# Optimization experiments

Hardware: AMD Instinct MI355X
Metric: run time of the kernel (lower is better)

## Reference

```python
import jax, jax.numpy as jnp
import numpy as np

K = 40  # GravNetConv k (hardcoded in PFNet7.forward's conv1)

def lrelu(x):
    # LeakyReLU(negative_slope=0.5)
    return jnp.where(x >= 0, x, 0.5 * x)

def lin(x, W, b=None):
    y = x @ W
    return y + b if b is not None else y


def setup_inputs() -> dict:
    key = jax.random.key(0)
    ks = jax.random.split(key, 24)
    N = 16384
    inp = {}
    inp["x0"] = jax.random.normal(ks[0], (N, 12), jnp.float32)
    inp["ygen"] = jax.random.normal(ks[1], (N, 6), jnp.float32)
    inp["ycand"] = jax.random.normal(ks[2], (N, 6), jnp.float32)
    inp["ygen_id"] = jax.random.randint(ks[3], (N,), 0, 6)
    inp["ycand_id"] = jax.random.randint(ks[4], (N,), 0, 6)

    def lp(k, din, dout):  # torch Linear default init (uniform +/- 1/sqrt(fan_in))
        s = float(1.0 / np.sqrt(din))
        kw, kb = jax.random.split(k)
        W = jax.random.uniform(kw, (din, dout), jnp.float32, -s, s)
        b = jax.random.uniform(kb, (dout,), jnp.float32, -s, s)
        return W, b

    inp["n1W0"], inp["n1b0"] = lp(ks[5], 12, 64)
    inp["n1W1"], inp["n1b1"] = lp(ks[6], 64, 64)
    inp["n1W2"], inp["n1b2"] = lp(ks[7], 64, 12)
    # GravNetConv: lin_s (space, 8), lin_h (propagate, 22), lin_out (12 + 2*22 -> 64)
    inp["gWs"], inp["gbs"] = lp(ks[8], 12, 8)
    inp["gWh"], inp["gbh"] = lp(ks[9], 12, 22)
    inp["gWo"], inp["gbo"] = lp(ks[10], 56, 64)
    # GraphConv: lin_rel (with bias), lin_root (no bias, PyG convention)
    inp["c2Wrel"], inp["c2brel"] = lp(ks[11], 64, 64)
    inp["c2Wroot"] = lp(ks[12], 64, 64)[0]
    inp["n2W0"], inp["n2b0"] = lp(ks[13], 64, 126)
    inp["n2W1"], inp["n2b1"] = lp(ks[14], 126, 126)
    inp["n2W2"], inp["n2b2"] = lp(ks[15], 126, 126)
    inp["n2W3"], inp["n2b3"] = lp(ks[16], 126, 6)
    inp["n3W0"], inp["n3b0"] = lp(ks[17], 82, 126)
    inp["n3W1"], inp["n3b1"] = lp(ks[18], 126, 126)
    inp["n3W2"], inp["n3b2"] = lp(ks[19], 126, 126)
    inp["n3W3"], inp["n3b3"] = lp(ks[20], 126, 6)
    return inp


def reference(x0, ygen, ycand, ygen_id, ycand_id,
              n1W0, n1b0, n1W1, n1b1, n1W2, n1b2,
              gWs, gbs, gWh, gbh, gWo, gbo,
              c2Wrel, c2brel, c2Wroot,
              n2W0, n2b0, n2W1, n2b1, n2W2, n2b2, n2W3, n2b3,
              n3W0, n3b0, n3W1, n3b1, n3W2, n3b2, n3W3, n3b3):
    N = x0.shape[0]
    # nn1 encoder
    x = lrelu(lin(x0, n1W0, n1b0))
    x = lrelu(lin(x, n1W1, n1b1))
    x = lrelu(lin(x, n1W2, n1b2))            # [N,12]
    # ---- GravNetConv: dynamic kNN graph in learned 8-dim space ----
    s = lin(x, gWs, gbs)                     # [N,8] spatial coords
    h = lin(x, gWh, gbh)                     # [N,22] propagated features
    sq = jnp.sum(s * s, axis=1)
    d2 = sq[:, None] + sq[None, :] - 2.0 * (s @ s.T)   # [N,N] squared dists
    ar = jnp.arange(N)
    d2 = d2.at[ar, ar].set(jnp.inf)          # knn_graph loop=False: no self edges
    negd2, idx = jax.lax.top_k(-d2, K)       # [N,K] k nearest neighbors
    w = jnp.exp(10.0 * negd2)                # edge_weight = exp(-10 * d^2)
    msg = h[idx] * w[..., None]              # [N,K,22] gathered messages
    agg = jnp.concatenate([msg.mean(axis=1), msg.max(axis=1)], axis=-1)  # [N,44]
    x = lin(jnp.concatenate([agg, x], axis=-1), gWo, gbo)  # [N,64]
    # ---- GraphConv on the same kNN graph (add-aggregation, edge-weighted) ----
    nbr = jnp.sum(x[idx] * w[..., None], axis=1)  # [N,64]
    x = lin(nbr, c2Wrel, c2brel) + x @ c2Wroot     # [N,64]
    # nn2: class id head
    y = lrelu(lin(x, n2W0, n2b0))
    y = lrelu(lin(y, n2W1, n2b1))
    y = lrelu(lin(y, n2W2, n2b2))
    cand_ids = lrelu(lin(y, n2W3, n2b3))     # [N,6]
    z = jnp.concatenate([x, cand_ids, x0], axis=-1)  # [N,82]
    z = lrelu(lin(z, n3W0, n3b0))
    z = lrelu(lin(z, n3W1, n3b1))
    z = lrelu(lin(z, n3W2, n3b2))
    cand_p4 = lrelu(lin(z, n3W3, n3b3))      # [N,6]
    return (cand_ids, cand_p4, ygen_id, ygen, ycand_id, ycand)
```

## Files before the change

### kernel.cpp

```cpp
#include <hip/hip_runtime.h>
#include <math.h>

static constexpr int KNN = 40;

__device__ __forceinline__ float lrelu_f(float v){ return v >= 0.f ? v : 0.5f*v; }

typedef _Float16 half8 __attribute__((ext_vector_type(8)));
typedef float    f32x4 __attribute__((ext_vector_type(4)));

__device__ __forceinline__ void gload16(const void* g, void* l){
    __builtin_amdgcn_global_load_lds((const __attribute__((address_space(1))) void*)g,
                                     (__attribute__((address_space(3))) void*)l, 16, 0, 0);
}

#define PAD_OFF_GWS   0
#define PAD_OFF_GWH   192
#define PAD_OFF_N1W2  576
#define PAD_OFF_N2W3  1600
#define PAD_OFF_N3W3  3616
#define PAD_TOTAL     5632

#define T_N2W0  0
#define T_N2W1  8192
#define T_N2W2  24576
#define T_N3W0  40960
#define T_N3W1  53248
#define T_N3W2  69632
#define T_TOTAL 86016

__global__ void pad_all(const float* gWs,const float* gWh,const float* n1W2,
                        const float* n2W3,const float* n3W3,
                        const float* n2W0,const float* n2W1,const float* n2W2,
                        const float* n3W0,const float* n3W1,const float* n3W2,
                        float* __restrict__ wp, _Float16* __restrict__ wt)
{
    int i = blockIdx.x*blockDim.x + threadIdx.x;
    if (i < PAD_TOTAL) {
        const float* src; int cols, sh, off;
        if      (i < PAD_OFF_GWH)  { src=gWs;  cols=8;  sh=4; off=PAD_OFF_GWS;  }
        else if (i < PAD_OFF_N1W2) { src=gWh;  cols=22; sh=5; off=PAD_OFF_GWH;  }
        else if (i < PAD_OFF_N2W3) { src=n1W2; cols=12; sh=4; off=PAD_OFF_N1W2; }
        else if (i < PAD_OFF_N3W3) { src=n2W3; cols=6;  sh=4; off=PAD_OFF_N2W3; }
        else                       { src=n3W3; cols=6;  sh=4; off=PAD_OFF_N3W3; }
        int li = i - off;
        int r = li >> sh, c = li & ((1<<sh)-1);
        wp[i] = (c < cols) ? src[r*cols + c] : 0.f;
        return;
    }
    int j = i - PAD_TOTAL;
    if (j >= T_TOTAL) return;
    const float* src; int KP, K, off;
    if      (j < T_N2W1) { src=n2W0; KP=64;  K=64;  off=T_N2W0; }
    else if (j < T_N2W2) { src=n2W1; KP=128; K=126; off=T_N2W1; }
    else if (j < T_N3W0) { src=n2W2; KP=128; K=126; off=T_N2W2; }
    else if (j < T_N3W1) { src=n3W0; KP=96;  K=82;  off=T_N3W0; }
    else if (j < T_N3W2) { src=n3W1; KP=128; K=126; off=T_N3W1; }
    else                 { src=n3W2; KP=128; K=126; off=T_N3W2; }
    int li = j - off;
    int n = li / KP, k = li - n*KP;
    float v = (n < 126 && k < K) ? src[k*126 + n] : 0.f;
    wt[j] = (_Float16)v;
}

template<int K, int NOUT, int WPITCH, bool RELU, int NTH>
__device__ __forceinline__
void lin8(const float* __restrict__ Xs, int xpitch,
          const float* __restrict__ W, const float* __restrict__ Bv,
          float* __restrict__ Y, int ypitch, int tid)
{
    constexpr int NP  = ((NOUT+7)/8)*8;
    constexpr int NCG = NP/8;
    constexpr int NW  = NTH/64;
    const int lane = tid & 63;
    for (int g0 = tid >> 6; g0 < NCG; g0 += NW) {
        const int cg = __builtin_amdgcn_readfirstlane(g0);
        float acc[8];
        #pragma unroll
        for (int j=0;j<8;++j){ int c=cg*8+j; acc[j] = (c < NOUT) ? Bv[c] : 0.f; }
        const float* xrow = &Xs[(long)lane*xpitch];
        const float* wp = &W[cg*8];
        #pragma unroll 4
        for (int k=0;k<K;++k){
            const float xv = xrow[k];
            const float4* w4 = reinterpret_cast<const float4*>(wp + (long)k*WPITCH);
            float4 a = w4[0], b = w4[1];
            acc[0]=fmaf(xv,a.x,acc[0]); acc[1]=fmaf(xv,a.y,acc[1]);
            acc[2]=fmaf(xv,a.z,acc[2]); acc[3]=fmaf(xv,a.w,acc[3]);
            acc[4]=fmaf(xv,b.x,acc[4]); acc[5]=fmaf(xv,b.y,acc[5]);
            acc[6]=fmaf(xv,b.z,acc[6]); acc[7]=fmaf(xv,b.w,acc[7]);
        }
        #pragma unroll
        for (int j=0;j<8;++j){
            int c = cg*8 + j;
            if (c < NOUT){ float v = acc[j]; if (RELU) v = lrelu_f(v); Y[(long)lane*ypitch + c] = v; }
        }
    }
    __syncthreads();
}

template<int K, int NOUT, int WPITCH, int NTH>
__device__ __forceinline__
void lin8_dual(const float* __restrict__ Xs, int xp, const float* __restrict__ X2s, int xp2,
               const float* __restrict__ W, const float* __restrict__ Bv, const float* __restrict__ W2,
               float* __restrict__ Y, int ypitch, int tid)
{
    constexpr int NP  = ((NOUT+7)/8)*8;
    constexpr int NCG = NP/8;
    constexpr int NW  = NTH/64;
    const int lane = tid & 63;
    for (int g0 = tid >> 6; g0 < NCG; g0 += NW) {
        const int cg = __builtin_amdgcn_readfirstlane(g0);
        float acc[8];
        #pragma unroll
        for (int j=0;j<8;++j){ int c=cg*8+j; acc[j] = (c < NOUT) ? Bv[c] : 0.f; }
        {
            const float* xrow = &Xs[(long)lane*xp];
            const float* wp = &W[cg*8];
            #pragma unroll 4
            for (int k=0;k<K;++k){
                const float xv = xrow[k];
                const float4* w4 = reinterpret_cast<const float4*>(wp + (long)k*WPITCH);
                float4 a = w4[0], b = w4[1];
                acc[0]=fmaf(xv,a.x,acc[0]); acc[1]=fmaf(xv,a.y,acc[1]);
                acc[2]=fmaf(xv,a.z,acc[2]); acc[3]=fmaf(xv,a.w,acc[3]);
                acc[4]=fmaf(xv,b.x,acc[4]); acc[5]=fmaf(xv,b.y,acc[5]);
                acc[6]=fmaf(xv,b.z,acc[6]); acc[7]=fmaf(xv,b.w,acc[7]);
            }
        }
        {
            const float* xrow = &X2s[(long)lane*xp2];
            const float* wp = &W2[cg*8];
            #pragma unroll 4
            for (int k=0;k<K;++k){
                const float xv = xrow[k];
                const float4* w4 = reinterpret_cast<const float4*>(wp + (long)k*WPITCH);
                float4 a = w4[0], b = w4[1];
                acc[0]=fmaf(xv,a.x,acc[0]); acc[1]=fmaf(xv,a.y,acc[1]);
                acc[2]=fmaf(xv,a.z,acc[2]); acc[3]=fmaf(xv,a.w,acc[3]);
                acc[4]=fmaf(xv,b.x,acc[4]); acc[5]=fmaf(xv,b.y,acc[5]);
                acc[6]=fmaf(xv,b.z,acc[6]); acc[7]=fmaf(xv,b.w,acc[7]);
            }
        }
        #pragma unroll
        for (int j=0;j<8;++j){
            int c = cg*8 + j;
            if (c < NOUT) Y[(long)lane*ypitch + c] = acc[j];
        }
    }
    __syncthreads();
}

__global__ __launch_bounds__(256)
void f1_encoder(const float* __restrict__ x0, const float* __restrict__ wp,
                const float* n1W0,const float* n1b0,const float* n1W1,const float* n1b1,
                const float* n1b2, const float* gbs, const float* gbh,
                float* __restrict__ x12g,
                _Float16* __restrict__ SA16, _Float16* __restrict__ SB16 ,
                float* __restrict__ hg )
{
    __shared__ float A1[64*65], A2[64*65], Ss[64*9];
    const int tid = threadIdx.x;
    const long row0 = (long)blockIdx.x*64;
    lin8<12,64,64,true,256>(x0+row0*12,12, n1W0, n1b0, A1,65, tid);
    lin8<64,64,64,true,256>(A1,65, n1W1, n1b1, A2,65, tid);
    lin8<64,12,16,true,256>(A2,65, wp+PAD_OFF_N1W2, n1b2, A1,13, tid);
    for (int i=tid;i<64*12;i+=256){ int r=i/12,c=i-r*12; x12g[(row0+r)*12+c]=A1[r*13+c]; }
    lin8<12,8,16,false,256>(A1,13, wp+PAD_OFF_GWS, gbs, Ss,9, tid);
    lin8<12,22,32,false,256>(A1,13, wp+PAD_OFF_GWH, gbh, hg+row0*32,32, tid);
    if (tid < 64) {
        const long node = row0 + tid;
        float sv[8]; float nq = 0.f;
        #pragma unroll
        for (int k=0;k<8;++k){ float v=Ss[tid*9+k]; sv[k]=v; nq=fmaf(v,v,nq); }
        _Float16 ch[8], clo[8];
        #pragma unroll
        for (int k=0;k<8;++k){ ch[k]=(_Float16)sv[k]; clo[k]=(_Float16)(sv[k]-(float)ch[k]); }
        _Float16 nh = (_Float16)nq, nl = (_Float16)(nq-(float)nh);
        const _Float16 one = (_Float16)1.f, zero = (_Float16)0.f;
        half8 a0,a1,a2,b0,b2;
        #pragma unroll
        for (int k=0;k<8;++k){
            a0[k]=ch[k]; a1[k]=clo[k]; a2[k]=ch[k];
            b0[k]=(_Float16)(-2.f*(float)ch[k]);
            b2[k]=(_Float16)(-2.f*(float)clo[k]);
        }
        half8 a3 = {nh, nl, one, one, zero, zero, zero, zero};
        half8 b3 = {one, one, nh, nl, zero, zero, zero, zero};
        half8* ap = (half8*)&SA16[(size_t)node*32];
        ap[0]=a0; ap[1]=a1; ap[2]=a2; ap[3]=a3;
        half8* bp = (half8*)&SB16[(size_t)node*40];
        bp[0]=b0; bp[1]=b0; bp[2]=b2; bp[3]=b3;
        bp[4]=half8{zero,zero,zero,zero,zero,zero,zero,zero};
    }
}

template<int C>
__device__ __forceinline__ unsigned dpp_umin(unsigned x){
    unsigned y = (unsigned)__builtin_amdgcn_update_dpp((int)x, (int)x, C, 0xf, 0xf, false);
    return x < y ? x : y;
}
__device__ __forceinline__ unsigned wave_umin64(unsigned x){
    x = dpp_umin<0x111>(x);
    x = dpp_umin<0x112>(x);
    x = dpp_umin<0x114>(x);
    x = dpp_umin<0x118>(x);
    x = dpp_umin<0x142>(x);
    x = dpp_umin<0x143>(x);
    return x;
}
__device__ __forceinline__ unsigned med3_u32(unsigned a, unsigned b, unsigned c){
    unsigned d;
    asm("v_med3_u32 %0, %1, %2, %3" : "=v"(d) : "v"(a), "v"(b), "v"(c));
    return d;
}

__global__ __launch_bounds__(512)
void knn_scan(const _Float16* __restrict__ SA, const _Float16* __restrict__ SB,
              unsigned* __restrict__ part, int N)
{
    __shared__ __align__(16) _Float16 SBl[2][256*40];
    const int tid  = threadIdx.x;
    const int lane = tid & 63;
    const int w    = tid >> 6;
    const int g    = w >> 2, qt = w & 3;
    const int col  = lane & 15, kg = lane >> 4;
    const int qg   = blockIdx.x >> 1, half = blockIdx.x & 1;
    const int qb   = qg*32 + g*16;
    const int qtile = qb >> 8;
    const int rhs0  = (qb & 255) + kg*4;
    const int T0 = half*32;

    half8 afrag = *(const half8*)&SA[(size_t)(qb + col)*32 + kg*8];
    unsigned s0[4], s1[4];
    #pragma unroll
    for (int r=0;r<4;++r){ s0[r]=0xFFFFFFFFu; s1[r]=0xFFFFFFFFu; }

    {
        const char* gp = (const char*)(SB + (size_t)T0*256*40);
        gload16(gp + (size_t)tid*16,        &SBl[0][(size_t)tid*8]);
        gload16(gp + (size_t)(tid+512)*16,  &SBl[0][(size_t)(tid+512)*8]);
        if (tid < 256) gload16(gp + (size_t)(tid+1024)*16, &SBl[0][(size_t)(tid+1024)*8]);
    }
    __syncthreads();
    #pragma unroll 1
    for (int t = T0; t < T0+32; ++t) {
        const int cur = t & 1;
        if (t+1 < T0+32) {
            const char* gp = (const char*)(SB + (size_t)(t+1)*256*40);
            _Float16* lp = SBl[cur^1];
            gload16(gp + (size_t)tid*16,        &lp[(size_t)tid*8]);
            gload16(gp + (size_t)(tid+512)*16,  &lp[(size_t)(tid+512)*8]);
            if (tid < 256) gload16(gp + (size_t)(tid+1024)*16, &lp[(size_t)(tid+1024)*8]);
        }
        const _Float16* tb = SBl[cur];
        if (t != qtile) {
            #pragma unroll
            for (int c3=0;c3<4;++c3){
                const int cl_ = (qt*4+c3)*16 + col;
                half8 b = *(const half8*)&tb[cl_*40 + kg*8];
                f32x4 acc = {0.f,0.f,0.f,0.f};
                acc = __builtin_amdgcn_mfma_f32_16x16x32_f16(afrag, b, acc, 0, 0, 0);
                const unsigned ib = (unsigned)((t<<8)|cl_);
                #pragma unroll
                for (int r=0;r<4;++r){
                    float d2 = fmaxf(acc[r], 0.f);
                    unsigned key = (__float_as_uint(d2) & 0xFFFFC000u) | ib;
                    unsigned lo = s0[r] < key ? s0[r] : key;
                    s1[r] = med3_u32(s0[r], s1[r], key);
                    s0[r] = lo;
                }
            }
        } else {
            #pragma unroll
            for (int c3=0;c3<4;++c3){
                const int cl_ = (qt*4+c3)*16 + col;
                half8 b = *(const half8*)&tb[cl_*40 + kg*8];
                f32x4 acc = {0.f,0.f,0.f,0.f};
                acc = __builtin_amdgcn_mfma_f32_16x16x32_f16(afrag, b, acc, 0, 0, 0);
                const unsigned ib = (unsigned)((t<<8)|cl_);
                #pragma unroll
                for (int r=0;r<4;++r){
                    float d2 = fmaxf(acc[r], 0.f);
                    unsigned key = (__float_as_uint(d2) & 0xFFFFC000u) | ib;
                    if (cl_ == rhs0 + r) key = 0xFFFFFFFFu;
                    unsigned lo = s0[r] < key ? s0[r] : key;
                    s1[r] = med3_u32(s0[r], s1[r], key);
                    s0[r] = lo;
                }
            }
        }
        __syncthreads();
    }

    #pragma unroll
    for (int r=0;r<4;++r){
        const long q = (long)qg*32 + g*16 + kg*4 + r;
        unsigned* pp = &part[((size_t)q*2 + half)*128 + qt*32 + col*2];
        pp[0] = s0[r]; pp[1] = s1[r];
    }
}

__global__ __launch_bounds__(512)
void knn_merge(const unsigned* __restrict__ part,
               int* __restrict__ idx_out, float* __restrict__ w_out)
{
    const int lane = threadIdx.x & 63, w = threadIdx.x >> 6;
    const long q = (long)blockIdx.x*8 + w;
    const uint4 kk = *reinterpret_cast<const uint4*>(&part[(size_t)q*256 + lane*4]);
    unsigned k0=kk.x, k1=kk.y, k2=kk.z, k3=kk.w;
    unsigned saved = 0;
    #pragma unroll 1
    for (int p=0;p<KNN;++p){
        unsigned a = k0 < k1 ? k0 : k1;
        unsigned b = k2 < k3 ? k2 : k3;
        unsigned lmin = a < b ? a : b;
        unsigned red = wave_umin64(lmin);
        unsigned gm = (unsigned)__builtin_amdgcn_readlane((int)red, 63);
        unsigned long long bal = __ballot(lmin == gm);
        int owner = __ffsll((long long)bal) - 1;
        if (lane == owner){
            if      (k0 == gm) k0 = 0xFFFFFFFFu;
            else if (k1 == gm) k1 = 0xFFFFFFFFu;
            else if (k2 == gm) k2 = 0xFFFFFFFFu;
            else               k3 = 0xFFFFFFFFu;
        }
        if (lane == p) saved = gm;
    }
    if (lane < KNN){
        idx_out[q*KNN + lane] = (int)(saved & 16383u);
        const float d2 = __uint_as_float(saved & 0xFFFFC000u);
        w_out[q*KNN + lane] = expf(-10.f*d2);
    }
}

__global__ __launch_bounds__(512)
void f2_agg(const float* __restrict__ hg , const int* __restrict__ idx,
            const float* __restrict__ wgt, const float* __restrict__ x12g,
            const float* gWo, const float* gbo, float* __restrict__ xg)
{
    __shared__ int   IDs[64*40];
    __shared__ float Wt[64*40];
    __shared__ float AGG[64*57];
    const int tid = threadIdx.x;
    const long row0 = (long)blockIdx.x*64;
    for (int i=tid;i<64*40;i+=512){ int r=i/40,k=i-r*40;
        IDs[i]=idx[(row0+r)*40+k]; Wt[i]=wgt[(row0+r)*40+k]; }
    for (int i=tid;i<64*12;i+=512){ int r=i/12,c=i-r*12; AGG[r*57+44+c]=x12g[(row0+r)*12+c]; }
    __syncthreads();
    {
        const int r = tid & 63, g = tid >> 6;
        const int f0 = g*4;
        const int nf = (f0 < 22) ? ((22-f0) < 4 ? (22-f0) : 4) : 0;
        float sm[4], mx[4];
        #pragma unroll
        for (int u=0;u<4;++u){ sm[u]=0.f; mx[u]=-INFINITY; }
        if (nf > 0) {
            #pragma unroll 1
            for (int k=0;k<40;++k){
                int j = IDs[r*40+k]; float wv = Wt[r*40+k];
                float4 h0 = *reinterpret_cast<const float4*>(&hg[(long)j*32 + f0]);
                float hv[4] = {h0.x,h0.y,h0.z,h0.w};
                #pragma unroll
                for (int u=0;u<4;++u){ float m = hv[u]*wv; sm[u]+=m; mx[u]=fmaxf(mx[u],m); }
            }
            #pragma unroll
            for (int u=0;u<4;++u) if (u<nf){ AGG[r*57+f0+u]=sm[u]*(1.f/40.f); AGG[r*57+22+f0+u]=mx[u]; }
        }
    }
    __syncthreads();
    lin8<56,64,64,false,512>(AGG,57, gWo, gbo, xg+row0*64,64, tid);
}

__global__ __launch_bounds__(512)
void f3_graphconv(const float* __restrict__ xgin, const int* __restrict__ idx,
                  const float* __restrict__ wgt,
                  const float* c2Wrel, const float* c2brel, const float* c2Wroot,
                  float* __restrict__ xc)
{
    __shared__ int   IDs[64*40];
    __shared__ float Wt[64*40];
    __shared__ float NB[64*65], XGs[64*65];
    const int tid = threadIdx.x;
    const long row0 = (long)blockIdx.x*64;
    for (int i=tid;i<64*40;i+=512){ int r=i/40,k=i-r*40;
        IDs[i]=idx[(row0+r)*40+k]; Wt[i]=wgt[(row0+r)*40+k]; }
    for (int i=tid;i<64*64;i+=512){ int r=i>>6,c=i&63; XGs[r*65+c]=xgin[(row0+r)*64+c]; }
    __syncthreads();
    {
        const int r = tid & 63, g = tid >> 6;
        float acc[8];
        #pragma unroll
        for (int j=0;j<8;++j) acc[j]=0.f;
        #pragma unroll 1
        for (int k=0;k<40;++k){
            int j = IDs[r*40+k]; float wv = Wt[r*40+k];
            const float4* xp = reinterpret_cast<const float4*>(&xgin[(long)j*64 + g*8]);
            float4 v0 = xp[0], v1 = xp[1];
            acc[0]=fmaf(v0.x,wv,acc[0]); acc[1]=fmaf(v0.y,wv,acc[1]);
            acc[2]=fmaf(v0.z,wv,acc[2]); acc[3]=fmaf(v0.w,wv,acc[3]);
            acc[4]=fmaf(v1.x,wv,acc[4]); acc[5]=fmaf(v1.y,wv,acc[5]);
            acc[6]=fmaf(v1.z,wv,acc[6]); acc[7]=fmaf(v1.w,wv,acc[7]);
        }
        #pragma unroll
        for (int j=0;j<8;++j) NB[r*65 + g*8 + j] = acc[j];
    }
    __syncthreads();
    lin8_dual<64,64,64,512>(NB,65, XGs,65, c2Wrel,c2brel,c2Wroot, xc+row0*64,64, tid);
}

template<int KP>
__device__ __forceinline__
void mfma_layer(const _Float16* __restrict__ Xl, const _Float16* __restrict__ WTg,
                _Float16* __restrict__ Wl,
                const float* __restrict__ Bv, _Float16* __restrict__ Yl, int tid)
{
    {
        const half8* src = reinterpret_cast<const half8*>(WTg);
        half8* dst = reinterpret_cast<half8*>(Wl);
        constexpr int CHUNKS = 128*KP/8;
        #pragma unroll
        for (int i = tid; i < CHUNKS; i += 1024) dst[i] = src[i];
    }
    __syncthreads();
    const int lane = tid & 63;
    const int wid  = __builtin_amdgcn_readfirstlane(tid >> 6);
    const int m   = wid & 3;
    const int nb  = wid >> 2;
    const int c15 = lane & 15;
    const int kg  = lane >> 4;
    f32x4 acc0 = {0.f,0.f,0.f,0.f};
    f32x4 acc1 = {0.f,0.f,0.f,0.f};
    const _Float16* xb = &Xl[(m*16 + c15)*136];
    const _Float16* w0 = &Wl[(nb*16 + c15)*KP];
    const _Float16* w1 = &Wl[((nb+4)*16 + c15)*KP];
    #pragma unroll
    for (int ks = 0; ks < KP/32; ++ks) {
        const int kb = kg*8 + ks*32;
        half8 a  = *reinterpret_cast<const half8*>(&xb[kb]);
        half8 b0 = *reinterpret_cast<const half8*>(&w0[kb]);
        half8 b1 = *reinterpret_cast<const half8*>(&w1[kb]);
        acc0 = __builtin_amdgcn_mfma_f32_16x16x32_f16(a, b0, acc0, 0, 0, 0);
        acc1 = __builtin_amdgcn_mfma_f32_16x16x32_f16(a, b1, acc1, 0, 0, 0);
    }
    const int drow = m*16 + kg*4;
    const int c0 = nb*16 + c15;
    const int c1 = (nb+4)*16 + c15;
    #pragma unroll
    for (int r = 0; r < 4; ++r) {
        float v0 = (c0 < 126) ? lrelu_f(acc0[r] + Bv[c0]) : 0.f;
        float v1 = (c1 < 126) ? lrelu_f(acc1[r] + Bv[c1]) : 0.f;
        Yl[(drow+r)*136 + c0] = (_Float16)v0;
        Yl[(drow+r)*136 + c1] = (_Float16)v1;
    }
    __syncthreads();
}

__device__ __forceinline__
void lin_out6h(const _Float16* __restrict__ Xs, const float* __restrict__ Wp,
               float* __restrict__ Wl6, const float* __restrict__ Bv,
               float* __restrict__ Y, int ypitch, int tid)
{
    for (int i = tid; i < 126*8; i += 1024) {
        int k = i >> 3, c = i & 7;
        Wl6[i] = Wp[k*16 + c];
    }
    __syncthreads();
    if (tid < 64*6) {
        const int r = tid / 6, c = tid - r*6;
        float acc = Bv[c];
        const _Float16* xrow = &Xs[r*136];
        #pragma unroll 4
        for (int k=0;k<126;++k) acc = fmaf((float)xrow[k], Wl6[k*8+c], acc);
        Y[(long)r*ypitch + c] = lrelu_f(acc);
    }
    __syncthreads();
}

__global__ __launch_bounds__(1024)
void f45_mfma(const float* __restrict__ xc, const float* __restrict__ x0,
              const float* __restrict__ wp, const _Float16* __restrict__ wt,
              const float* A_b0,const float* A_b1,const float* A_b2,const float* A_b3,
              const float* B_b0,const float* B_b1,const float* B_b2,const float* B_b3,
              float* __restrict__ outIds, float* __restrict__ outP4)
{
    __shared__ __align__(16) _Float16 bufA[64*136];
    __shared__ __align__(16) _Float16 bufB[64*136];
    __shared__ __align__(16) _Float16 Wl[128*128];
    __shared__ float IDS[64*6];
    const int tid = threadIdx.x;
    const long row0 = (long)blockIdx.x*64;
    for (int i=tid;i<64*64;i+=1024){ int r=i>>6,c=i&63;
        bufA[r*136+c] = (_Float16)xc[(row0+r)*64+c]; }
    __syncthreads();
    mfma_layer<64>(bufA, wt+T_N2W0, Wl, A_b0, bufB, tid);
    mfma_layer<128>(bufB, wt+T_N2W1, Wl, A_b1, bufA, tid);
    mfma_layer<128>(bufA, wt+T_N2W2, Wl, A_b2, bufB, tid);
    lin_out6h(bufB, wp+PAD_OFF_N2W3, (float*)Wl, A_b3, IDS, 6, tid);
    for (int i=tid;i<64*6;i+=1024){ int r=i/6,c=i-r*6; outIds[(row0+r)*6+c]=IDS[i]; }
    for (int i=tid;i<64*96;i+=1024){
        int r=i/96, c=i-r*96;
        float v;
        if (c < 64)      v = xc[(row0+r)*64 + c];
        else if (c < 70) v = IDS[r*6 + (c-64)];
        else if (c < 82) v = x0[(row0+r)*12 + (c-70)];
        else             v = 0.f;
        bufA[r*136+c] = (_Float16)v;
    }
    __syncthreads();
    mfma_layer<96>(bufA, wt+T_N3W0, Wl, B_b0, bufB, tid);
    mfma_layer<128>(bufB, wt+T_N3W1, Wl, B_b1, bufA, tid);
    mfma_layer<128>(bufA, wt+T_N3W2, Wl, B_b2, bufB, tid);
    lin_out6h(bufB, wp+PAD_OFF_N3W3, (float*)Wl, B_b3, outP4+row0*6, 6, tid);
}

__global__ void copyout_kernel(const int* __restrict__ gid, const float* __restrict__ gy,
                               const int* __restrict__ cid, const float* __restrict__ cy,
                               float* __restrict__ out, int N)
{
    long i = (long)blockIdx.x*blockDim.x + threadIdx.x;
    long n = N;
    if (i < n)            out[12*n + i]         = (float)gid[i];
    else if (i < 7*n)     out[13*n + (i - n)]   = gy[i - n];
    else if (i < 8*n)     out[19*n + (i - 7*n)] = (float)cid[i - 7*n];
    else if (i < 14*n)    out[20*n + (i - 8*n)] = cy[i - 8*n];
}

extern "C" void kernel_launch(void* const* d_in, const int* in_sizes, int n_in,
                              void* d_out, int out_size, void* d_ws, size_t ws_size,
                              hipStream_t stream)
{
    const float* x0     = (const float*)d_in[0];
    const float* ygen   = (const float*)d_in[1];
    const float* ycand  = (const float*)d_in[2];
    const int*   ygenid = (const int*)d_in[3];
    const int*   ycandid= (const int*)d_in[4];
    const float* n1W0=(const float*)d_in[5],  *n1b0=(const float*)d_in[6];
    const float* n1W1=(const float*)d_in[7],  *n1b1=(const float*)d_in[8];
    const float* n1W2=(const float*)d_in[9],  *n1b2=(const float*)d_in[10];
    const float* gWs =(const float*)d_in[11], *gbs =(const float*)d_in[12];
    const float* gWh =(const float*)d_in[13], *gbh =(const float*)d_in[14];
    const float* gWo =(const float*)d_in[15], *gbo =(const float*)d_in[16];
    const float* c2Wrel=(const float*)d_in[17], *c2brel=(const float*)d_in[18];
    const float* c2Wroot=(const float*)d_in[19];
    const float* n2W0=(const float*)d_in[20], *n2b0=(const float*)d_in[21];
    const float* n2W1=(const float*)d_in[22], *n2b1=(const float*)d_in[23];
    const float* n2W2=(const float*)d_in[24], *n2b2=(const float*)d_in[25];
    const float* n2W3=(const float*)d_in[26], *n2b3=(const float*)d_in[27];
    const float* n3W0=(const float*)d_in[28], *n3b0=(const float*)d_in[29];
    const float* n3W1=(const float*)d_in[30], *n3b1=(const float*)d_in[31];
    const float* n3W2=(const float*)d_in[32], *n3b2=(const float*)d_in[33];
    const float* n3W3=(const float*)d_in[34], *n3b3=(const float*)d_in[35];

    const int N = in_sizes[0] / 12;
    float* ws = (float*)d_ws;
    size_t off = 0;
    auto alloc = [&](size_t cnt){ float* p = ws + off; off += cnt; return p; };
    float* padw = alloc(PAD_TOTAL);
    _Float16* wt16 = (_Float16*)alloc((T_TOTAL+1)/2 + 8);
    float* x12  = alloc((size_t)N*12);
    _Float16* SA16 = (_Float16*)alloc((size_t)N*16);
    _Float16* SB16 = (_Float16*)alloc((size_t)N*20);
    float* h    = alloc((size_t)N*32);
    unsigned* part = (unsigned*)alloc((size_t)N*256);
    int*   idxb = (int*)alloc((size_t)N*KNN);
    float* wb   = alloc((size_t)N*KNN);
    float* xg   = alloc((size_t)N*64);
    float* xc   = alloc((size_t)N*64);
    (void)ws_size; (void)n_in; (void)out_size;

    float* outF = (float*)d_out;
    const int GB = N / 64;

    pad_all<<<(PAD_TOTAL+T_TOTAL+255)/256,256,0,stream>>>(gWs,gWh,n1W2,n2W3,n3W3,
                                                          n2W0,n2W1,n2W2,n3W0,n3W1,n3W2,
                                                          padw, wt16);
    f1_encoder<<<GB,256,0,stream>>>(x0, padw, n1W0,n1b0, n1W1,n1b1, n1b2,
                                    gbs, gbh, x12, SA16, SB16, h);
    knn_scan<<<(N/32)*2, 512, 0, stream>>>(SA16, SB16, part, N);
    knn_merge<<<N/8, 512, 0, stream>>>(part, idxb, wb);
    f2_agg<<<GB,512,0,stream>>>(h, idxb, wb, x12, gWo, gbo, xg);
    f3_graphconv<<<GB,512,0,stream>>>(xg, idxb, wb, c2Wrel, c2brel, c2Wroot, xc);
    f45_mfma<<<GB,1024,0,stream>>>(xc, x0, padw, wt16,
                                   n2b0,n2b1,n2b2,n2b3, n3b0,n3b1,n3b2,n3b3,
                                   outF, outF + (size_t)N*6);
    copyout_kernel<<<(14*N+255)/256,256,0,stream>>>(ygenid, ygen, ycandid, ycand, outF, N);
}
```

Baseline: 215.4 us.

## Fuse GraphConv into MLP-head kernel and widen encoder blocks to 512 threads

Merges the GraphConv kernel into the fused MLP-head kernel, so the GraphConv output stays in shared memory as XCs and is never written to or read back from global memory. The two phases share one aliased shared-memory union, and the neighbor gather is split across 1024 threads with 4 features each. This removes one kernel launch and an N×64 global round trip. Separately, the encoder kernel's launch bound and block size rise from 256 to 512 threads. The risks are lower occupancy from roughly 86KB of shared memory per 1024-thread block, and an extra barrier to protect the aliased buffers.

```diff
diff --git a/kernel.cpp b/kernel.cpp
--- a/kernel.cpp
+++ b/kernel.cpp
@@ -150,7 +150,7 @@
     __syncthreads();
 }
 
-__global__ __launch_bounds__(256)
+__global__ __launch_bounds__(512)
 void f1_encoder(const float* __restrict__ x0, const float* __restrict__ wp,
                 const float* n1W0,const float* n1b0,const float* n1W1,const float* n1b1,
                 const float* n1b2, const float* gbs, const float* gbh,
@@ -161,12 +161,12 @@
     __shared__ float A1[64*65], A2[64*65], Ss[64*9];
     const int tid = threadIdx.x;
     const long row0 = (long)blockIdx.x*64;
-    lin8<12,64,64,true,256>(x0+row0*12,12, n1W0, n1b0, A1,65, tid);
-    lin8<64,64,64,true,256>(A1,65, n1W1, n1b1, A2,65, tid);
-    lin8<64,12,16,true,256>(A2,65, wp+PAD_OFF_N1W2, n1b2, A1,13, tid);
-    for (int i=tid;i<64*12;i+=256){ int r=i/12,c=i-r*12; x12g[(row0+r)*12+c]=A1[r*13+c]; }
-    lin8<12,8,16,false,256>(A1,13, wp+PAD_OFF_GWS, gbs, Ss,9, tid);
-    lin8<12,22,32,false,256>(A1,13, wp+PAD_OFF_GWH, gbh, hg+row0*32,32, tid);
+    lin8<12,64,64,true,512>(x0+row0*12,12, n1W0, n1b0, A1,65, tid);
+    lin8<64,64,64,true,512>(A1,65, n1W1, n1b1, A2,65, tid);
+    lin8<64,12,16,true,512>(A2,65, wp+PAD_OFF_N1W2, n1b2, A1,13, tid);
+    for (int i=tid;i<64*12;i+=512){ int r=i/12,c=i-r*12; x12g[(row0+r)*12+c]=A1[r*13+c]; }
+    lin8<12,8,16,false,512>(A1,13, wp+PAD_OFF_GWS, gbs, Ss,9, tid);
+    lin8<12,22,32,false,512>(A1,13, wp+PAD_OFF_GWH, gbh, hg+row0*32,32, tid);
     if (tid < 64) {
         const long node = row0 + tid;
         float sv[8]; float nq = 0.f;
@@ -371,43 +371,6 @@
     lin8<56,64,64,false,512>(AGG,57, gWo, gbo, xg+row0*64,64, tid);
 }
 
-__global__ __launch_bounds__(512)
-void f3_graphconv(const float* __restrict__ xgin, const int* __restrict__ idx,
-                  const float* __restrict__ wgt,
-                  const float* c2Wrel, const float* c2brel, const float* c2Wroot,
-                  float* __restrict__ xc)
-{
-    __shared__ int   IDs[64*40];
-    __shared__ float Wt[64*40];
-    __shared__ float NB[64*65], XGs[64*65];
-    const int tid = threadIdx.x;
-    const long row0 = (long)blockIdx.x*64;
-    for (int i=tid;i<64*40;i+=512){ int r=i/40,k=i-r*40;
-        IDs[i]=idx[(row0+r)*40+k]; Wt[i]=wgt[(row0+r)*40+k]; }
-    for (int i=tid;i<64*64;i+=512){ int r=i>>6,c=i&63; XGs[r*65+c]=xgin[(row0+r)*64+c]; }
-    __syncthreads();
-    {
-        const int r = tid & 63, g = tid >> 6;
-        float acc[8];
-        #pragma unroll
-        for (int j=0;j<8;++j) acc[j]=0.f;
-        #pragma unroll 1
-        for (int k=0;k<40;++k){
-            int j = IDs[r*40+k]; float wv = Wt[r*40+k];
-            const float4* xp = reinterpret_cast<const float4*>(&xgin[(long)j*64 + g*8]);
-            float4 v0 = xp[0], v1 = xp[1];
-            acc[0]=fmaf(v0.x,wv,acc[0]); acc[1]=fmaf(v0.y,wv,acc[1]);
-            acc[2]=fmaf(v0.z,wv,acc[2]); acc[3]=fmaf(v0.w,wv,acc[3]);
-            acc[4]=fmaf(v1.x,wv,acc[4]); acc[5]=fmaf(v1.y,wv,acc[5]);
-            acc[6]=fmaf(v1.z,wv,acc[6]); acc[7]=fmaf(v1.w,wv,acc[7]);
-        }
-        #pragma unroll
-        for (int j=0;j<8;++j) NB[r*65 + g*8 + j] = acc[j];
-    }
-    __syncthreads();
-    lin8_dual<64,64,64,512>(NB,65, XGs,65, c2Wrel,c2brel,c2Wroot, xc+row0*64,64, tid);
-}
-
 template<int KP>
 __device__ __forceinline__
 void mfma_layer(const _Float16* __restrict__ Xl, const _Float16* __restrict__ WTg,
@@ -477,31 +440,61 @@
 }
 
 __global__ __launch_bounds__(1024)
-void f45_mfma(const float* __restrict__ xc, const float* __restrict__ x0,
-              const float* __restrict__ wp, const _Float16* __restrict__ wt,
-              const float* A_b0,const float* A_b1,const float* A_b2,const float* A_b3,
-              const float* B_b0,const float* B_b1,const float* B_b2,const float* B_b3,
-              float* __restrict__ outIds, float* __restrict__ outP4)
-{
-    __shared__ __align__(16) _Float16 bufA[64*136];
-    __shared__ __align__(16) _Float16 bufB[64*136];
-    __shared__ __align__(16) _Float16 Wl[128*128];
-    __shared__ float IDS[64*6];
+void f345(const float* __restrict__ xgin, const int* __restrict__ idx,
+          const float* __restrict__ wgt,
+          const float* c2Wrel, const float* c2brel, const float* c2Wroot,
+          const float* __restrict__ x0,
+          const float* __restrict__ wp, const _Float16* __restrict__ wt,
+          const float* A_b0,const float* A_b1,const float* A_b2,const float* A_b3,
+          const float* B_b0,const float* B_b1,const float* B_b2,const float* B_b3,
+          float* __restrict__ outIds, float* __restrict__ outP4)
+{
+    __shared__ float XCs[64*65];
+    __shared__ __align__(16) char uni[69120];
+    int*   IDs = (int*)uni;
+    float* Wt  = (float*)(uni+10240);
+    float* NB  = (float*)(uni+20480);
+    float* XGs = (float*)(uni+37120);
+    _Float16* bufA = (_Float16*)uni;
+    _Float16* bufB = (_Float16*)(uni+17408);
+    _Float16* Wl   = (_Float16*)(uni+34816);
+    float*    IDS6 = (float*)(uni+67584);
+
     const int tid = threadIdx.x;
     const long row0 = (long)blockIdx.x*64;
+    for (int i=tid;i<64*40;i+=1024){ int r=i/40,k=i-r*40;
+        IDs[i]=idx[(row0+r)*40+k]; Wt[i]=wgt[(row0+r)*40+k]; }
+    for (int i=tid;i<64*64;i+=1024){ int r=i>>6,c=i&63; XGs[r*65+c]=xgin[(row0+r)*64+c]; }
+    __syncthreads();
+    {
+        const int r = tid & 63, g = tid >> 6;
+        float acc[4] = {0.f,0.f,0.f,0.f};
+        #pragma unroll 1
+        for (int k=0;k<40;++k){
+            int j = IDs[r*40+k]; float wv = Wt[r*40+k];
+            float4 v = *reinterpret_cast<const float4*>(&xgin[(long)j*64 + g*4]);
+            acc[0]=fmaf(v.x,wv,acc[0]); acc[1]=fmaf(v.y,wv,acc[1]);
+            acc[2]=fmaf(v.z,wv,acc[2]); acc[3]=fmaf(v.w,wv,acc[3]);
+        }
+        __syncthreads();
+        #pragma unroll
+        for (int j=0;j<4;++j) NB[r*65 + g*4 + j] = acc[j];
+    }
+    __syncthreads();
+    lin8_dual<64,64,64,1024>(NB,65, XGs,65, c2Wrel,c2brel,c2Wroot, XCs,65, tid);
     for (int i=tid;i<64*64;i+=1024){ int r=i>>6,c=i&63;
-        bufA[r*136+c] = (_Float16)xc[(row0+r)*64+c]; }
+        bufA[r*136+c] = (_Float16)XCs[r*65+c]; }
     __syncthreads();
     mfma_layer<64>(bufA, wt+T_N2W0, Wl, A_b0, bufB, tid);
     mfma_layer<128>(bufB, wt+T_N2W1, Wl, A_b1, bufA, tid);
     mfma_layer<128>(bufA, wt+T_N2W2, Wl, A_b2, bufB, tid);
-    lin_out6h(bufB, wp+PAD_OFF_N2W3, (float*)Wl, A_b3, IDS, 6, tid);
-    for (int i=tid;i<64*6;i+=1024){ int r=i/6,c=i-r*6; outIds[(row0+r)*6+c]=IDS[i]; }
+    lin_out6h(bufB, wp+PAD_OFF_N2W3, (float*)Wl, A_b3, IDS6, 6, tid);
+    for (int i=tid;i<64*6;i+=1024){ int r=i/6,c=i-r*6; outIds[(row0+r)*6+c]=IDS6[i]; }
     for (int i=tid;i<64*96;i+=1024){
         int r=i/96, c=i-r*96;
         float v;
-        if (c < 64)      v = xc[(row0+r)*64 + c];
-        else if (c < 70) v = IDS[r*6 + (c-64)];
+        if (c < 64)      v = XCs[r*65 + c];
+        else if (c < 70) v = IDS6[r*6 + (c-64)];
         else if (c < 82) v = x0[(row0+r)*12 + (c-70)];
         else             v = 0.f;
         bufA[r*136+c] = (_Float16)v;
@@ -565,7 +558,6 @@
     int*   idxb = (int*)alloc((size_t)N*KNN);
     float* wb   = alloc((size_t)N*KNN);
     float* xg   = alloc((size_t)N*64);
-    float* xc   = alloc((size_t)N*64);
     (void)ws_size; (void)n_in; (void)out_size;
 
     float* outF = (float*)d_out;
@@ -574,14 +566,13 @@
     pad_all<<<(PAD_TOTAL+T_TOTAL+255)/256,256,0,stream>>>(gWs,gWh,n1W2,n2W3,n3W3,
                                                           n2W0,n2W1,n2W2,n3W0,n3W1,n3W2,
                                                           padw, wt16);
-    f1_encoder<<<GB,256,0,stream>>>(x0, padw, n1W0,n1b0, n1W1,n1b1, n1b2,
+    f1_encoder<<<GB,512,0,stream>>>(x0, padw, n1W0,n1b0, n1W1,n1b1, n1b2,
                                     gbs, gbh, x12, SA16, SB16, h);
     knn_scan<<<(N/32)*2, 512, 0, stream>>>(SA16, SB16, part, N);
     knn_merge<<<N/8, 512, 0, stream>>>(part, idxb, wb);
     f2_agg<<<GB,512,0,stream>>>(h, idxb, wb, x12, gWo, gbo, xg);
-    f3_graphconv<<<GB,512,0,stream>>>(xg, idxb, wb, c2Wrel, c2brel, c2Wroot, xc);
-    f45_mfma<<<GB,1024,0,stream>>>(xc, x0, padw, wt16,
-                                   n2b0,n2b1,n2b2,n2b3, n3b0,n3b1,n3b2,n3b3,
-                                   outF, outF + (size_t)N*6);
+    f345<<<GB,1024,0,stream>>>(xg, idxb, wb, c2Wrel, c2brel, c2Wroot, x0, padw, wt16,
+                               n2b0,n2b1,n2b2,n2b3, n3b0,n3b1,n3b2,n3b3,
+                               outF, outF + (size_t)N*6);
     copyout_kernel<<<(14*N+255)/256,256,0,stream>>>(ygenid, ygen, ycandid, ycand, outF, N);
 }
```

Result: faster. 204.4 us (-5.1%).
